# Kernel tuning notes

Hardware: AMD Instinct MI355X
Metric: run time of the kernel (lower is better)

## Reference

```python
import jax, jax.numpy as jnp
import numpy as np

NUM_HEADS = 8
D_HEAD = 64
ATTENTION_WINDOW = 512


def alibi_bias(num_heads, q_len, k_len):
    # ALiBi slopes for power-of-2 number of heads (Press et al. 2021).
    start = 2.0 ** (-(2.0 ** -(np.log2(num_heads) - 3.0)))
    slopes = jnp.asarray([start * (start ** i) for i in range(num_heads)],
                         dtype=jnp.float32)  # [H]
    rel = jnp.arange(q_len)[:, None] - jnp.arange(k_len)[None, :]  # [t, T]
    # Bidirectional ALiBi: bias = -slope * |i - j|
    return -slopes[:, None, None] * jnp.abs(rel).astype(jnp.float32)  # [H, t, T]


def sliding_window_mask(seq_len, window):
    # Attend to tokens within window//2 on each side; even window -> window+1.
    if window % 2 == 0:
        window += 1
    half = window // 2
    idx = jnp.arange(seq_len)
    return jnp.abs(idx[:, None] - idx[None, :]) <= half  # [S, S] bool


def setup_inputs() -> dict:
    key = jax.random.key(0)
    ks = jax.random.split(key, 6)
    B, S, E = 2, 4096, 512
    HD = NUM_HEADS * D_HEAD
    s_in = 1.0 / np.sqrt(E)
    s_out = 1.0 / np.sqrt(HD)
    return {
        'inputs_q': jax.random.normal(ks[0], (B, S, E), jnp.float32),
        'inputs_kv': jax.random.normal(ks[1], (B, S, E), jnp.float32),
        'w_q': jax.random.normal(ks[2], (E, HD), jnp.float32) * s_in,
        'w_k': jax.random.normal(ks[3], (E, HD), jnp.float32) * s_in,
        'w_v': jax.random.normal(ks[4], (E, HD), jnp.float32) * s_in,
        'w_o': jax.random.normal(ks[5], (HD, E), jnp.float32) * s_out,
    }


def reference(inputs_q, inputs_kv, w_q, w_k, w_v, w_o):
    B, S, E = inputs_q.shape
    H, D = NUM_HEADS, D_HEAD
    q = (inputs_q @ w_q).reshape(B, S, H, D)
    k = (inputs_kv @ w_k).reshape(B, S, H, D)
    v = (inputs_kv @ w_v).reshape(B, S, H, D)
    # scores: [B, H, t, T]
    att = jnp.einsum('bthd,bThd->bhtT', q, k) * (1.0 / jnp.sqrt(jnp.float32(D)))
    att = att + alibi_bias(H, S, S)[None]
    mask = sliding_window_mask(S, ATTENTION_WINDOW)
    att = jnp.where(mask[None, None], att, jnp.finfo(jnp.float32).min)
    p = jax.nn.softmax(att, axis=-1)
    out = jnp.einsum('bhtT,bThd->bthd', p, v).reshape(B, S, H * D)
    return out @ w_o
```

## Files before the change

kernel.cpp:

```cpp
#include <hip/hip_runtime.h>

#define S_LEN  4096
#define NH     8
#define DH     64
#define EMB    512
#define HDIM   512
#define HALF_W 256
#define BATCH  2
#define M_ROWS (BATCH * S_LEN)

typedef __attribute__((ext_vector_type(8))) short bf16x8;
typedef __attribute__((ext_vector_type(4))) float f32x4;

#define LOG2E 1.44269504088896f

__device__ __forceinline__ float b2f(unsigned short u) {
    union { unsigned int i; float f; } v; v.i = ((unsigned int)u) << 16; return v.f;
}
__device__ __forceinline__ unsigned short f2b(float f) {
    unsigned int x = __float_as_uint(f);
    unsigned int r = (x + 0x7fffu + ((x >> 16) & 1u)) >> 16;
    return (unsigned short)r;
}
__device__ __forceinline__ unsigned int f2bpk(float a, float b) {
    return ((__float_as_uint(a) + 0x8000u) >> 16) |
           ((__float_as_uint(b) + 0x8000u) & 0xffff0000u);
}
__device__ __forceinline__ void unpack2(unsigned int u, float* d) {
    d[0] = b2f((unsigned short)(u & 0xffffu));
    d[1] = b2f((unsigned short)(u >> 16));
}
union FragU { uint4 u; bf16x8 f; };
__device__ __forceinline__ bf16x8 ldfrag(const unsigned short* p) {
    FragU x; x.u = *(const uint4*)p; return x.f;
}

__device__ __forceinline__ void async16(const unsigned short* g, unsigned short* l) {
    __builtin_amdgcn_global_load_lds(
        (__attribute__((address_space(1))) void*)const_cast<unsigned short*>(g),
        (__attribute__((address_space(3))) void*)l, 16, 0, 0);
}

__device__ __forceinline__ int detect_flag(const unsigned short* __restrict__ xq) {
    __shared__ int s_flag;
    if (threadIdx.x == 0) s_flag = 0;
    __syncthreads();
    uint4 u = *(const uint4*)(xq + threadIdx.x * 8);
    const unsigned short* us = (const unsigned short*)&u;
    int bad = 0;
#pragma unroll
    for (int i = 0; i < 8; ++i) {
        float v = b2f(us[i]);
        if (!(fabsf(v) < 1.0e6f)) bad = 1;
    }
    if (__any(bad) && (threadIdx.x & 63) == 0) atomicOr(&s_flag, 1);
    __syncthreads();
    return s_flag;
}

__global__ __launch_bounds__(256) void prep(
    const void* __restrict__ xq,
    const void* __restrict__ w0, const void* __restrict__ w1,
    const void* __restrict__ w2, const void* __restrict__ w3,
    unsigned short* __restrict__ Wt)
{
    const int flag = detect_flag((const unsigned short*)xq);
    const int blk = blockIdx.x;
    __shared__ float t[32][33];
    const int z = blk >> 8, idx = blk & 255;
    const void* src = (z == 0) ? w0 : (z == 1) ? w1 : (z == 2) ? w2 : w3;
    unsigned short* dst = Wt + (size_t)z * EMB * EMB;
    const int n0 = (idx & 15) << 5, k0 = (idx >> 4) << 5;
    const int kk = threadIdx.x >> 3;
    const int n4 = (threadIdx.x & 7) << 2;
    if (flag) {
        float4 v = *(const float4*)((const float*)src + (size_t)(k0 + kk) * EMB + n0 + n4);
        t[kk][n4] = v.x; t[kk][n4 + 1] = v.y; t[kk][n4 + 2] = v.z; t[kk][n4 + 3] = v.w;
    } else {
        uint2 u = *(const uint2*)((const unsigned short*)src + (size_t)(k0 + kk) * EMB + n0 + n4);
        unpack2(u.x, &t[kk][n4]); unpack2(u.y, &t[kk][n4 + 2]);
    }
    __syncthreads();
    const int nn = threadIdx.x >> 3;
    const int ks = (threadIdx.x & 7) << 2;
    uint2 pk;
    pk.x = (unsigned int)f2b(t[ks + 0][nn]) | ((unsigned int)f2b(t[ks + 1][nn]) << 16);
    pk.y = (unsigned int)f2b(t[ks + 2][nn]) | ((unsigned int)f2b(t[ks + 3][nn]) << 16);
    *(uint2*)(dst + (size_t)(n0 + nn) * EMB + k0 + ks) = pk;
}

__device__ __forceinline__ void mgemm_core7(
    const void* __restrict__ Av, int aFp32,
    const unsigned short* __restrict__ Bt,
    int m0, f32x4 (*acc)[4],
    unsigned short (*A_lds)[32], unsigned short (*B_lds)[32])
{
    const int tid  = threadIdx.x;
    const int lane = tid & 63;
    const int w    = tid >> 6;
    const int wm   = (w >> 1) << 6;
    const int wn   = (w & 1) << 6;
    const int qcol = lane & 15;
    const int quad = lane >> 4;

    const int arow = (w << 4) + (lane >> 2);
    const int acol = (lane & 3) << 3;

    const unsigned short* gB = Bt + (size_t)arow * EMB + acol;
    unsigned short* lA0 = &A_lds[arow][acol];
    unsigned short* lA1 = &A_lds[64 + arow][acol];
    unsigned short* lB0 = &B_lds[arow][acol];
    unsigned short* lB1 = &B_lds[64 + arow][acol];
    const size_t half = (size_t)64 * EMB;

    const float* gAf = (const float*)Av + (size_t)(m0 + arow) * EMB + acol;
    const unsigned short* gAb = (const unsigned short*)Av + (size_t)(m0 + arow) * EMB + acol;

    for (int k0 = 0; k0 < EMB; k0 += 32) {
        __syncthreads();
        if (aFp32) {
            float4 a0 = *(const float4*)(gAf + k0);
            float4 a1 = *(const float4*)(gAf + k0 + 4);
            float4 a2 = *(const float4*)(gAf + half + k0);
            float4 a3 = *(const float4*)(gAf + half + k0 + 4);
            async16(gB + k0, lB0);
            async16(gB + half + k0, lB1);
            uint4 u0, u1;
            u0.x = f2bpk(a0.x, a0.y); u0.y = f2bpk(a0.z, a0.w);
            u0.z = f2bpk(a1.x, a1.y); u0.w = f2bpk(a1.z, a1.w);
            u1.x = f2bpk(a2.x, a2.y); u1.y = f2bpk(a2.z, a2.w);
            u1.z = f2bpk(a3.x, a3.y); u1.w = f2bpk(a3.z, a3.w);
            *(uint4*)lA0 = u0;
            *(uint4*)lA1 = u1;
        } else {
            async16(gAb + k0, lA0);
            async16(gAb + half + k0, lA1);
            async16(gB + k0, lB0);
            async16(gB + half + k0, lB1);
        }
        __syncthreads();

        bf16x8 af[4], bf[4];
#pragma unroll
        for (int i = 0; i < 4; ++i) af[i] = ldfrag(&A_lds[wm + (i << 4) + qcol][quad * 8]);
#pragma unroll
        for (int j = 0; j < 4; ++j) bf[j] = ldfrag(&B_lds[wn + (j << 4) + qcol][quad * 8]);
#pragma unroll
        for (int i = 0; i < 4; ++i)
#pragma unroll
            for (int j = 0; j < 4; ++j)
                acc[i][j] = __builtin_amdgcn_mfma_f32_16x16x32_bf16(af[i], bf[j], acc[i][j], 0, 0, 0);
    }
}

__global__ __launch_bounds__(256) void gemm_qkv(
    const void* __restrict__ xq, const void* __restrict__ xkv,
    const unsigned short* __restrict__ Wt,
    unsigned short* __restrict__ Qb, unsigned short* __restrict__ Kb,
    unsigned short* __restrict__ Vtb)
{
    const int flag = detect_flag((const unsigned short*)xq);
    __shared__ __align__(16) unsigned short A_lds[128][32];
    __shared__ __align__(16) unsigned short B_lds[128][32];
    const int blk = blockIdx.x;
    const int xcd = blk & 7, idx = blk >> 3;
    const int mi = idx / 12, ni = idx - mi * 12;
    const int m0 = ((xcd << 3) + mi) << 7;
    const int n0 = ni << 7;

    const void* A = (n0 < 512) ? xq : xkv;
    const unsigned short* Bt = Wt + (size_t)n0 * EMB;

    f32x4 acc[4][4];
#pragma unroll
    for (int i = 0; i < 4; ++i)
#pragma unroll
        for (int j = 0; j < 4; ++j) acc[i][j] = (f32x4){0.f, 0.f, 0.f, 0.f};

    mgemm_core7(A, flag, Bt, m0, acc, A_lds, B_lds);

    const int lane = threadIdx.x & 63, w = threadIdx.x >> 6;
    const int wm = (w >> 1) << 6, wn = (w & 1) << 6;
    const int qcol = lane & 15, quad = lane >> 4;
    const int mode = (n0 < 512) ? 0 : (n0 < 1024) ? 1 : 2;
    const float qscale = 0.125f * LOG2E;
#pragma unroll
    for (int ms = 0; ms < 4; ++ms)
#pragma unroll
        for (int ns = 0; ns < 4; ++ns)
#pragma unroll
            for (int r = 0; r < 4; ++r) {
                const int m = m0 + wm + (ms << 4) + (quad << 2) + r;
                const int n = n0 + wn + (ns << 4) + qcol;
                if (mode == 0) {
                    Qb[(size_t)m * HDIM + n] = f2b(acc[ms][ns][r] * qscale);
                } else if (mode == 1) {
                    Kb[(size_t)m * HDIM + (n - 512)] = f2b(acc[ms][ns][r]);
                } else {
                    const int hd = n - 1024;
                    const int bb = m >> 12, s = m & (S_LEN - 1);
                    const int hh = hd >> 6, d = hd & 63;
                    Vtb[((size_t)((bb * NH + hh) * DH + d)) * S_LEN + s] = f2b(acc[ms][ns][r]);
                }
            }
}

__device__ __forceinline__ void mgemm_core4(
    const unsigned short* __restrict__ A, const unsigned short* __restrict__ Bt,
    int m0, f32x4 (*acc)[2],
    unsigned short (*A_lds)[64], unsigned short (*B_lds)[64])
{
    const int tid  = threadIdx.x;
    const int lane = tid & 63;
    const int w    = tid >> 6;
    const int wm   = (w >> 1) << 6;
    const int wn   = (w & 1) << 5;
    const int qcol = lane & 15;
    const int quad = lane >> 4;
    const int srow = tid >> 3;
    const int sp   = tid & 7;

    for (int k0 = 0; k0 < EMB; k0 += 64) {
        __syncthreads();
#pragma unroll
        for (int i = 0; i < 4; ++i) {
            const int row  = (i << 5) + srow;
            const int gcol = ((sp ^ (row & 7)) << 3);
            async16(A + (size_t)(m0 + row) * EMB + k0 + gcol, &A_lds[row][sp << 3]);
        }
#pragma unroll
        for (int i = 0; i < 2; ++i) {
            const int row  = (i << 5) + srow;
            const int gcol = ((sp ^ (row & 7)) << 3);
            async16(Bt + (size_t)row * EMB + k0 + gcol, &B_lds[row][sp << 3]);
        }
        __syncthreads();

#pragma unroll
        for (int kh = 0; kh < 2; ++kh) {
            bf16x8 af[4], bf[2];
#pragma unroll
            for (int i = 0; i < 4; ++i) {
                const int row = wm + (i << 4) + qcol;
                const int p   = ((kh << 2) + quad) ^ (row & 7);
                af[i] = ldfrag(&A_lds[row][p << 3]);
            }
#pragma unroll
            for (int j = 0; j < 2; ++j) {
                const int row = wn + (j << 4) + qcol;
                const int p   = ((kh << 2) + quad) ^ (row & 7);
                bf[j] = ldfrag(&B_lds[row][p << 3]);
            }
#pragma unroll
            for (int i = 0; i < 4; ++i)
#pragma unroll
                for (int j = 0; j < 2; ++j)
                    acc[i][j] = __builtin_amdgcn_mfma_f32_16x16x32_bf16(af[i], bf[j], acc[i][j], 0, 0, 0);
        }
    }
}

__global__ __launch_bounds__(256) void gemm_out(
    const void* __restrict__ xq,
    const unsigned short* __restrict__ A, const unsigned short* __restrict__ Bt,
    void* __restrict__ C)
{
    const int flag = detect_flag((const unsigned short*)xq);
    __shared__ __align__(16) unsigned short A_lds[128][64];
    __shared__ __align__(16) unsigned short B_lds[64][64];
    const int blk = blockIdx.x;
    const int xcd = blk & 7, idx = blk >> 3;
    const int mi = idx >> 3, ni = idx & 7;
    const int m0 = ((xcd << 3) + mi) << 7;
    const int n0 = ni << 6;

    f32x4 acc[4][2];
#pragma unroll
    for (int i = 0; i < 4; ++i)
#pragma unroll
        for (int j = 0; j < 2; ++j) acc[i][j] = (f32x4){0.f, 0.f, 0.f, 0.f};

    mgemm_core4(A, Bt + (size_t)n0 * EMB, m0, acc, A_lds, B_lds);

    const int lane = threadIdx.x & 63, w = threadIdx.x >> 6;
    const int wm = (w >> 1) << 6, wn = (w & 1) << 5;
    const int qcol = lane & 15, quad = lane >> 4;
#pragma unroll
    for (int ms = 0; ms < 4; ++ms)
#pragma unroll
        for (int ns = 0; ns < 2; ++ns)
#pragma unroll
            for (int r = 0; r < 4; ++r) {
                const int m = m0 + wm + (ms << 4) + (quad << 2) + r;
                const int n = n0 + wn + (ns << 4) + qcol;
                const float v = acc[ms][ns][r];
                if (flag) ((float*)C)[(size_t)m * HDIM + n] = v;
                else      ((unsigned short*)C)[(size_t)m * HDIM + n] = f2b(v);
            }
}

__device__ __forceinline__ void attn_issue(
    const unsigned short* __restrict__ Kg, const unsigned short* __restrict__ Vt,
    int b, int h, int j0,
    unsigned short (*Kb)[64], unsigned short (*Vb)[64], int srow, int sp)
{
#pragma unroll
    for (int i = 0; i < 2; ++i) {
        const int row  = (i << 5) + srow;
        const int gseg = (sp ^ (row & 7)) << 3;
        const int jc = min(max(j0 + row, 0), S_LEN - 1);
        async16(Kg + (size_t)(b * S_LEN + jc) * HDIM + h * DH + gseg, &Kb[row][sp << 3]);
        const int js = min(max(j0 + gseg, 0), S_LEN - 8);
        async16(Vt + ((size_t)((b * NH + h) * DH + row)) * S_LEN + js, &Vb[row][sp << 3]);
    }
}

__global__ __launch_bounds__(256) void attn_mfma(
    const unsigned short* __restrict__ Q,
    const unsigned short* __restrict__ Kg,
    const unsigned short* __restrict__ Vt,
    unsigned short* __restrict__ O)
{
    __shared__ __align__(16) unsigned short K_lds[2][64][64];
    __shared__ __align__(16) unsigned short V_lds[2][64][64];
    __shared__ __align__(16) unsigned short P_lds[4][32][72];

    const int tid  = threadIdx.x;
    const int lane = tid & 63;
    const int w    = tid >> 6;
    const int blk  = blockIdx.x;
    const int bh   = blk >> 5;
    const int r5   = blk & 31;
    const int tile = ((r5 & 7) << 2) | (r5 >> 3);
    const int h    = bh & (NH - 1);
    const int b    = bh >> 3;
    const int t0   = tile << 7;
    const int tq0  = t0 + (w << 5);

    const int qcol = lane & 15;
    const int quad = lane >> 4;
    const float slope2 = LOG2E / (float)(2 << h);
    const float bias2  = 12.0f * LOG2E;

    bf16x8 qf[2][2];
#pragma unroll
    for (int qs = 0; qs < 2; ++qs) {
        const unsigned short* qrow =
            Q + (size_t)(b * S_LEN + tq0 + (qs << 4) + qcol) * HDIM + h * DH;
        qf[qs][0] = ldfrag(qrow + quad * 8);
        qf[qs][1] = ldfrag(qrow + 32 + quad * 8);
    }

    f32x4 Oacc[2][4];
#pragma unroll
    for (int qs = 0; qs < 2; ++qs)
#pragma unroll
        for (int i = 0; i < 4; ++i) Oacc[qs][i] = (f32x4){0.f, 0.f, 0.f, 0.f};
    float lsum[2] = {0.f, 0.f};

    const int srow = tid >> 3;
    const int sp   = tid & 7;

    attn_issue(Kg, Vt, b, h, t0 - HALF_W, K_lds[0], V_lds[0], srow, sp);

    for (int c = 0; c < 10; ++c) {
        const int j0 = t0 - HALF_W + (c << 6);
        __syncthreads();
        if (c < 9)
            attn_issue(Kg, Vt, b, h, j0 + 64,
                       K_lds[(c + 1) & 1], V_lds[(c + 1) & 1], srow, sp);
        const int bi = c & 1;

        if (j0 + 63 < tq0 - HALF_W || j0 > tq0 + 31 + HALF_W) continue;

#pragma unroll
        for (int qs = 0; qs < 2; ++qs) {
            const int qv = tq0 + (qs << 4) + qcol;
#pragma unroll
            for (int ks = 0; ks < 4; ++ks) {
                const int sj0 = j0 + (ks << 4);
                unsigned short* pdst = &P_lds[w][(qs << 4) + qcol][(ks << 4) + (quad << 2)];
                if (sj0 + 15 < tq0 + (qs << 4) - HALF_W ||
                    sj0 > tq0 + (qs << 4) + 15 + HALF_W) {
                    *(uint2*)pdst = (uint2){0u, 0u};
                    continue;
                }
                const int krow = (ks << 4) + qcol;
                const bf16x8 kf0 = ldfrag(&K_lds[bi][krow][(quad ^ (krow & 7)) << 3]);
                const bf16x8 kf1 = ldfrag(&K_lds[bi][krow][((4 + quad) ^ (krow & 7)) << 3]);
                f32x4 z = (f32x4){0.f, 0.f, 0.f, 0.f};
                z = __builtin_amdgcn_mfma_f32_16x16x32_bf16(kf0, qf[qs][0], z, 0, 0, 0);
                z = __builtin_amdgcn_mfma_f32_16x16x32_bf16(kf1, qf[qs][1], z, 0, 0, 0);
                float p[4];
#pragma unroll
                for (int r = 0; r < 4; ++r) {
                    const int j  = sj0 + (quad << 2) + r;
                    const int dd = qv - j;
                    const int ad = dd < 0 ? -dd : dd;
                    const bool ok = (ad <= HALF_W) && ((unsigned)j < (unsigned)S_LEN);
                    const float arg = fmaf(-slope2, (float)ad, z[r] - bias2);
                    const float e = exp2f(arg);
                    p[r] = ok ? e : 0.0f;
                    lsum[qs] += p[r];
                }
                uint2 pk;
                pk.x = f2bpk(p[0], p[1]);
                pk.y = f2bpk(p[2], p[3]);
                *(uint2*)pdst = pk;
            }
        }
#pragma unroll
        for (int qs = 0; qs < 2; ++qs) {
            const bf16x8 pf0 = ldfrag(&P_lds[w][(qs << 4) + qcol][quad * 8]);
            const bf16x8 pf1 = ldfrag(&P_lds[w][(qs << 4) + qcol][32 + quad * 8]);
#pragma unroll
            for (int ds = 0; ds < 4; ++ds) {
                const int vrow = (ds << 4) + qcol;
                const bf16x8 vf0 = ldfrag(&V_lds[bi][vrow][(quad ^ (vrow & 7)) << 3]);
                const bf16x8 vf1 = ldfrag(&V_lds[bi][vrow][((4 + quad) ^ (vrow & 7)) << 3]);
                Oacc[qs][ds] = __builtin_amdgcn_mfma_f32_16x16x32_bf16(vf0, pf0, Oacc[qs][ds], 0, 0, 0);
                Oacc[qs][ds] = __builtin_amdgcn_mfma_f32_16x16x32_bf16(vf1, pf1, Oacc[qs][ds], 0, 0, 0);
            }
        }
    }

#pragma unroll
    for (int qs = 0; qs < 2; ++qs) {
        float l = lsum[qs];
        l += __shfl_xor(l, 16, 64);
        l += __shfl_xor(l, 32, 64);
        const float rz = 1.0f / l;
        unsigned short* obase =
            O + (size_t)(b * S_LEN + tq0 + (qs << 4) + qcol) * HDIM + h * DH;
#pragma unroll
        for (int ds = 0; ds < 4; ++ds) {
            uint2 pk;
            pk.x = f2bpk(Oacc[qs][ds][0] * rz, Oacc[qs][ds][1] * rz);
            pk.y = f2bpk(Oacc[qs][ds][2] * rz, Oacc[qs][ds][3] * rz);
            *(uint2*)(obase + (ds << 4) + (quad << 2)) = pk;
        }
    }
}

extern "C" void kernel_launch(void* const* d_in, const int* in_sizes, int n_in,
                              void* d_out, int out_size, void* d_ws, size_t ws_size,
                              hipStream_t stream) {
    const void* xq  = d_in[0];
    const void* xkv = d_in[1];
    const void* wq  = d_in[2];
    const void* wk  = d_in[3];
    const void* wv  = d_in[4];
    const void* wo  = d_in[5];

    unsigned short* Qb  = (unsigned short*)((char*)d_ws + 256);
    unsigned short* Kb  = Qb  + (size_t)M_ROWS * HDIM;
    unsigned short* Vtb = Kb  + (size_t)M_ROWS * HDIM;
    unsigned short* Wt  = Vtb + (size_t)M_ROWS * HDIM;
    unsigned short* Wto = Wt + (size_t)3 * EMB * EMB;

    prep<<<1024, 256, 0, stream>>>(xq, wq, wk, wv, wo, Wt);
    gemm_qkv<<<768, 256, 0, stream>>>(xq, xkv, Wt, Qb, Kb, Vtb);
    attn_mfma<<<BATCH * NH * (S_LEN / 128), 256, 0, stream>>>(Qb, Kb, Vtb, Qb);
    gemm_out<<<512, 256, 0, stream>>>(xq, Qb, Wto, d_out);
}
```

Before: 183.2 us.

## Retile QKV GEMM to 128x64 tiles with K=64 steps and padded LDS

The QKV projection GEMM now uses 128x64 output tiles instead of 128x128, which doubles the grid to 1536 blocks. It steps K by 64 per iteration, with LDS rows padded to 72 elements to avoid bank conflicts. Global loads now go into registers before the barrier instead of through async copies, so the loads of the next tile can overlap. The goal is better occupancy and fewer synchronisations per K, at the cost of less B-tile reuse and twice as many reads of the A matrix.

```diff
diff --git a/kernel.cpp b/kernel.cpp
--- a/kernel.cpp
+++ b/kernel.cpp
@@ -89,67 +89,68 @@
     *(uint2*)(dst + (size_t)(n0 + nn) * EMB + k0 + ks) = pk;
 }
 
-__device__ __forceinline__ void mgemm_core7(
+__device__ __forceinline__ void mgemm_core8(
     const void* __restrict__ Av, int aFp32,
     const unsigned short* __restrict__ Bt,
-    int m0, f32x4 (*acc)[4],
-    unsigned short (*A_lds)[32], unsigned short (*B_lds)[32])
+    int m0, f32x4 (*acc)[2],
+    unsigned short (*A_lds)[72], unsigned short (*B_lds)[72])
 {
     const int tid  = threadIdx.x;
     const int lane = tid & 63;
     const int w    = tid >> 6;
     const int wm   = (w >> 1) << 6;
-    const int wn   = (w & 1) << 6;
+    const int wn   = (w & 1) << 5;
     const int qcol = lane & 15;
     const int quad = lane >> 4;
-
-    const int arow = (w << 4) + (lane >> 2);
-    const int acol = (lane & 3) << 3;
-
-    const unsigned short* gB = Bt + (size_t)arow * EMB + acol;
-    unsigned short* lA0 = &A_lds[arow][acol];
-    unsigned short* lA1 = &A_lds[64 + arow][acol];
-    unsigned short* lB0 = &B_lds[arow][acol];
-    unsigned short* lB1 = &B_lds[64 + arow][acol];
-    const size_t half = (size_t)64 * EMB;
-
-    const float* gAf = (const float*)Av + (size_t)(m0 + arow) * EMB + acol;
-    const unsigned short* gAb = (const unsigned short*)Av + (size_t)(m0 + arow) * EMB + acol;
-
-    for (int k0 = 0; k0 < EMB; k0 += 32) {
+    const int srow = tid >> 3;
+    const int sp   = tid & 7;
+
+    const float* gAf = (const float*)Av;
+    const unsigned short* gAb = (const unsigned short*)Av;
+
+    for (int it = 0; it < 8; ++it) {
+        const int k0 = it << 6;
+        uint4 ua[4], ub[2];
+        if (aFp32) {
+#pragma unroll
+            for (int i = 0; i < 4; ++i) {
+                const float* p = gAf + (size_t)(m0 + (i << 5) + srow) * EMB + k0 + (sp << 3);
+                float4 x = *(const float4*)p;
+                float4 y = *(const float4*)(p + 4);
+                ua[i].x = f2bpk(x.x, x.y); ua[i].y = f2bpk(x.z, x.w);
+                ua[i].z = f2bpk(y.x, y.y); ua[i].w = f2bpk(y.z, y.w);
+            }
+        } else {
+#pragma unroll
+            for (int i = 0; i < 4; ++i)
+                ua[i] = *(const uint4*)(gAb + (size_t)(m0 + (i << 5) + srow) * EMB + k0 + (sp << 3));
+        }
+#pragma unroll
+        for (int i = 0; i < 2; ++i)
+            ub[i] = *(const uint4*)(Bt + (size_t)((i << 5) + srow) * EMB + k0 + (sp << 3));
+
         __syncthreads();
-        if (aFp32) {
-            float4 a0 = *(const float4*)(gAf + k0);
-            float4 a1 = *(const float4*)(gAf + k0 + 4);
-            float4 a2 = *(const float4*)(gAf + half + k0);
-            float4 a3 = *(const float4*)(gAf + half + k0 + 4);
-            async16(gB + k0, lB0);
-            async16(gB + half + k0, lB1);
-            uint4 u0, u1;
-            u0.x = f2bpk(a0.x, a0.y); u0.y = f2bpk(a0.z, a0.w);
-            u0.z = f2bpk(a1.x, a1.y); u0.w = f2bpk(a1.z, a1.w);
-            u1.x = f2bpk(a2.x, a2.y); u1.y = f2bpk(a2.z, a2.w);
-            u1.z = f2bpk(a3.x, a3.y); u1.w = f2bpk(a3.z, a3.w);
-            *(uint4*)lA0 = u0;
-            *(uint4*)lA1 = u1;
-        } else {
-            async16(gAb + k0, lA0);
-            async16(gAb + half + k0, lA1);
-            async16(gB + k0, lB0);
-            async16(gB + half + k0, lB1);
-        }
+#pragma unroll
+        for (int i = 0; i < 4; ++i) *(uint4*)&A_lds[(i << 5) + srow][sp << 3] = ua[i];
+#pragma unroll
+        for (int i = 0; i < 2; ++i) *(uint4*)&B_lds[(i << 5) + srow][sp << 3] = ub[i];
         __syncthreads();
 
-        bf16x8 af[4], bf[4];
-#pragma unroll
-        for (int i = 0; i < 4; ++i) af[i] = ldfrag(&A_lds[wm + (i << 4) + qcol][quad * 8]);
-#pragma unroll
-        for (int j = 0; j < 4; ++j) bf[j] = ldfrag(&B_lds[wn + (j << 4) + qcol][quad * 8]);
-#pragma unroll
-        for (int i = 0; i < 4; ++i)
-#pragma unroll
-            for (int j = 0; j < 4; ++j)
-                acc[i][j] = __builtin_amdgcn_mfma_f32_16x16x32_bf16(af[i], bf[j], acc[i][j], 0, 0, 0);
+#pragma unroll
+        for (int kh = 0; kh < 2; ++kh) {
+            bf16x8 af[4], bf[2];
+#pragma unroll
+            for (int i = 0; i < 4; ++i)
+                af[i] = ldfrag(&A_lds[wm + (i << 4) + qcol][(kh << 5) + quad * 8]);
+#pragma unroll
+            for (int j = 0; j < 2; ++j)
+                bf[j] = ldfrag(&B_lds[wn + (j << 4) + qcol][(kh << 5) + quad * 8]);
+#pragma unroll
+            for (int i = 0; i < 4; ++i)
+#pragma unroll
+                for (int j = 0; j < 2; ++j)
+                    acc[i][j] = __builtin_amdgcn_mfma_f32_16x16x32_bf16(af[i], bf[j], acc[i][j], 0, 0, 0);
+        }
     }
 }
 
@@ -160,34 +161,34 @@
     unsigned short* __restrict__ Vtb)
 {
     const int flag = detect_flag((const unsigned short*)xq);
-    __shared__ __align__(16) unsigned short A_lds[128][32];
-    __shared__ __align__(16) unsigned short B_lds[128][32];
+    __shared__ __align__(16) unsigned short A_lds[128][72];
+    __shared__ __align__(16) unsigned short B_lds[64][72];
     const int blk = blockIdx.x;
     const int xcd = blk & 7, idx = blk >> 3;
-    const int mi = idx / 12, ni = idx - mi * 12;
+    const int mi = idx / 24, ni = idx - mi * 24;
     const int m0 = ((xcd << 3) + mi) << 7;
-    const int n0 = ni << 7;
+    const int n0 = ni << 6;
 
     const void* A = (n0 < 512) ? xq : xkv;
     const unsigned short* Bt = Wt + (size_t)n0 * EMB;
 
-    f32x4 acc[4][4];
+    f32x4 acc[4][2];
 #pragma unroll
     for (int i = 0; i < 4; ++i)
 #pragma unroll
-        for (int j = 0; j < 4; ++j) acc[i][j] = (f32x4){0.f, 0.f, 0.f, 0.f};
-
-    mgemm_core7(A, flag, Bt, m0, acc, A_lds, B_lds);
+        for (int j = 0; j < 2; ++j) acc[i][j] = (f32x4){0.f, 0.f, 0.f, 0.f};
+
+    mgemm_core8(A, flag, Bt, m0, acc, A_lds, B_lds);
 
     const int lane = threadIdx.x & 63, w = threadIdx.x >> 6;
-    const int wm = (w >> 1) << 6, wn = (w & 1) << 6;
+    const int wm = (w >> 1) << 6, wn = (w & 1) << 5;
     const int qcol = lane & 15, quad = lane >> 4;
-    const int mode = (n0 < 512) ? 0 : (n0 < 1024) ? 1 : 2;
+    const int mode = n0 >> 9;
     const float qscale = 0.125f * LOG2E;
 #pragma unroll
     for (int ms = 0; ms < 4; ++ms)
 #pragma unroll
-        for (int ns = 0; ns < 4; ++ns)
+        for (int ns = 0; ns < 2; ++ns)
 #pragma unroll
             for (int r = 0; r < 4; ++r) {
                 const int m = m0 + wm + (ms << 4) + (quad << 2) + r;
@@ -459,7 +460,7 @@
     unsigned short* Wto = Wt + (size_t)3 * EMB * EMB;
 
     prep<<<1024, 256, 0, stream>>>(xq, wq, wk, wv, wo, Wt);
-    gemm_qkv<<<768, 256, 0, stream>>>(xq, xkv, Wt, Qb, Kb, Vtb);
+    gemm_qkv<<<1536, 256, 0, stream>>>(xq, xkv, Wt, Qb, Kb, Vtb);
     attn_mfma<<<BATCH * NH * (S_LEN / 128), 256, 0, stream>>>(Qb, Kb, Vtb, Qb);
     gemm_out<<<512, 256, 0, stream>>>(xq, Qb, Wto, d_out);
 }
```

New measurement: 198.4 us. 1.08x slower.
